# Optimization experiments

Hardware: AMD Instinct MI355X
Metric: run time of the kernel (lower is better)

The kernel has to match this reference:

```python
import jax, jax.numpy as jnp
import numpy as np

B, L, INPUT_DIM = 2, 2048, 512
D_MODEL, N_HEAD, MLP_HIDDEN = 1024, 16, 4096
CONTEXT_LENGTH = 2048
EPS = 1e-5


def _layer_norm(x, w, b):
    mu = jnp.mean(x, axis=-1, keepdims=True)
    var = jnp.mean(jnp.square(x - mu), axis=-1, keepdims=True)
    return (x - mu) * jax.lax.rsqrt(var + EPS) * w + b


def setup_inputs() -> dict:
    key = jax.random.key(0)
    ks = jax.random.split(key, 12)
    s = 0.02
    return {
        "x": jax.random.normal(ks[0], (B, L, INPUT_DIM), dtype=jnp.float32),
        "wte_w": jax.random.normal(ks[1], (INPUT_DIM, D_MODEL), dtype=jnp.float32) * s,
        "wte_b": jnp.zeros((D_MODEL,), dtype=jnp.float32),
        "wpe": jax.random.normal(ks[2], (CONTEXT_LENGTH, D_MODEL), dtype=jnp.float32) * s,
        "ln1_w": jnp.ones((D_MODEL,), dtype=jnp.float32),
        "ln1_b": jnp.zeros((D_MODEL,), dtype=jnp.float32),
        "kq_w": jax.random.normal(ks[3], (D_MODEL, 2 * D_MODEL), dtype=jnp.float32) * s,
        "kq_b": jnp.zeros((2 * D_MODEL,), dtype=jnp.float32),
        "v_w": jax.random.normal(ks[4], (D_MODEL, D_MODEL), dtype=jnp.float32) * s,
        "v_b": jnp.zeros((D_MODEL,), dtype=jnp.float32),
        "ao_w": jax.random.normal(ks[5], (D_MODEL, D_MODEL), dtype=jnp.float32) * s,
        "ao_b": jnp.zeros((D_MODEL,), dtype=jnp.float32),
        "ln2_w": jnp.ones((D_MODEL,), dtype=jnp.float32),
        "ln2_b": jnp.zeros((D_MODEL,), dtype=jnp.float32),
        "fc_w": jax.random.normal(ks[6], (D_MODEL, MLP_HIDDEN), dtype=jnp.float32) * s,
        "fc_b": jnp.zeros((MLP_HIDDEN,), dtype=jnp.float32),
        "proj_w": jax.random.normal(ks[7], (MLP_HIDDEN, INPUT_DIM), dtype=jnp.float32) * s,
        "proj_b": jnp.zeros((INPUT_DIM,), dtype=jnp.float32),
    }


def reference(x, wte_w, wte_b, wpe, ln1_w, ln1_b, kq_w, kq_b, v_w, v_b,
              ao_w, ao_b, ln2_w, ln2_b, fc_w, fc_b, proj_w, proj_b):
    b, l, _ = x.shape
    hd = D_MODEL // N_HEAD
    # token "embedding" (linear) + learnable positional embedding
    h = x @ wte_w + wte_b + wpe[:l]                      # [B, L, D]
    hn = _layer_norm(h, ln1_w, ln1_b)                    # ln_1
    # attention (kq fused linear -> split gives k first, then q)
    kq = hn @ kq_w + kq_b                                # [B, L, 2D]
    k, q = kq[..., :D_MODEL], kq[..., D_MODEL:]
    v = hn @ v_w + v_b
    q = q.reshape(b, l, N_HEAD, hd).transpose(0, 2, 1, 3)  # [B, H, L, hd]
    k = k.reshape(b, l, N_HEAD, hd).transpose(0, 2, 1, 3)
    v = v.reshape(b, l, N_HEAD, hd).transpose(0, 2, 1, 3)
    scale = 1.0 / jnp.sqrt(jnp.asarray(hd, dtype=q.dtype))
    scores = jnp.einsum('bhqd,bhkd->bhqk', q, k) * scale  # [B, H, L, L]
    causal = jnp.tril(jnp.ones((l, l), dtype=bool))
    scores = jnp.where(causal, scores, jnp.asarray(-jnp.inf, dtype=scores.dtype))
    attn = jax.nn.softmax(scores, axis=-1)
    o = jnp.einsum('bhqk,bhkd->bhqd', attn, v)            # [B, H, L, hd]
    o = o.transpose(0, 2, 1, 3).reshape(b, l, D_MODEL)
    o = o @ ao_w + ao_b
    attn_out = hn + o                                     # residual recorded by Block
    xo = _layer_norm(attn_out, ln2_w, ln2_b)              # ln_2
    # MLP head to input_dim (exact GELU, matching torch nn.GELU default)
    out = jax.nn.gelu(xo @ fc_w + fc_b, approximate=False) @ proj_w + proj_b
    return (out, attn_out)
```

## Files before the change

### kernel.cpp

```cpp
#include <hip/hip_runtime.h>
#include <hip/hip_bf16.h>
#include <cmath>

#define D_MODEL   1024
#define N_HEAD    16
#define HEAD_DIM  64
#define SEQ_LEN   2048
#define NBATCH    2
#define M_TOTAL   (NBATCH * SEQ_LEN)
#define IN_DIM    512
#define MLP_HID   4096

typedef __attribute__((ext_vector_type(8))) short short8;
typedef __attribute__((ext_vector_type(4))) short short4v;
typedef __attribute__((ext_vector_type(4))) float floatx4;

typedef const __attribute__((address_space(1))) void* gas_ptr;
typedef __attribute__((address_space(3))) void* las_ptr;

__device__ __forceinline__ void async_copy16(const void* g, void* l) {
  __builtin_amdgcn_global_load_lds((gas_ptr)g, (las_ptr)l, 16, 0, 0);
}


__global__ __launch_bounds__(256) void k_convert_bf16(const float* __restrict__ in,
                                                      __hip_bfloat16* __restrict__ out,
                                                      int n4) {
  int i = blockIdx.x * 256 + threadIdx.x;
  if (i >= n4) return;
  float4 v = ((const float4*)in)[i];
  int base = i * 4;
  out[base + 0] = __float2bfloat16(v.x);
  out[base + 1] = __float2bfloat16(v.y);
  out[base + 2] = __float2bfloat16(v.z);
  out[base + 3] = __float2bfloat16(v.w);
}

__global__ __launch_bounds__(256) void k_reduce_proj(const __hip_bfloat16* __restrict__ part,
                                                     const float* __restrict__ bias,
                                                     float* __restrict__ out) {
  int i = blockIdx.x * 256 + threadIdx.x;
  const size_t SP = (size_t)M_TOTAL * IN_DIM / 4;
  float4 s = ((const float4*)bias)[i & (IN_DIM / 4 - 1)];
#pragma unroll
  for (int j = 0; j < 8; j++) {
    short4v v = ((const short4v*)part)[i + j * SP];
    s.x += __bfloat162float(((const __hip_bfloat16*)&v)[0]);
    s.y += __bfloat162float(((const __hip_bfloat16*)&v)[1]);
    s.z += __bfloat162float(((const __hip_bfloat16*)&v)[2]);
    s.w += __bfloat162float(((const __hip_bfloat16*)&v)[3]);
  }
  ((float4*)out)[i] = s;
}

__global__ __launch_bounds__(256) void k_transpose_bf16(const float* __restrict__ in,
                                                        __hip_bfloat16* __restrict__ out,
                                                        int K, int N) {
  __shared__ float tile[32][33];
  int n0 = blockIdx.x * 32, k0 = blockIdx.y * 32;
  int tx = threadIdx.x & 31, ty = threadIdx.x >> 5;
#pragma unroll
  for (int i = 0; i < 32; i += 8)
    tile[ty + i][tx] = in[(size_t)(k0 + ty + i) * N + n0 + tx];
  __syncthreads();
#pragma unroll
  for (int i = 0; i < 32; i += 8)
    out[(size_t)(n0 + ty + i) * K + k0 + tx] = __float2bfloat16(tile[tx][ty + i]);
}

__global__ __launch_bounds__(256) void k_transpose_v(const __hip_bfloat16* __restrict__ in,
                                                     __hip_bfloat16* __restrict__ out) {
  __shared__ __hip_bfloat16 t[64][72];
  int bh = blockIdx.y;
  int l0 = blockIdx.x * 64;
  in  += (size_t)bh * SEQ_LEN * HEAD_DIM;
  out += (size_t)bh * HEAD_DIM * SEQ_LEN;
  int tx = threadIdx.x & 7, ty = threadIdx.x >> 3;
#pragma unroll
  for (int i = 0; i < 64; i += 32) {
    short8 v = *(const short8*)(in + (size_t)(l0 + ty + i) * HEAD_DIM + tx * 8);
#pragma unroll
    for (int j = 0; j < 8; j++) t[ty + i][tx * 8 + j] = ((__hip_bfloat16*)&v)[j];
  }
  __syncthreads();
#pragma unroll
  for (int i = 0; i < 64; i += 32) {
    int d = ty + i;
    short8 o;
#pragma unroll
    for (int j = 0; j < 8; j++) ((__hip_bfloat16*)&o)[j] = t[tx * 8 + j][d];
    *(short8*)(out + (size_t)d * SEQ_LEN + l0 + tx * 8) = o;
  }
}


__global__ __launch_bounds__(256) void k_ln1_combine(const float* __restrict__ part,
                                                     const float* __restrict__ wb,
                                                     const float* __restrict__ wpe,
                                                     const float* __restrict__ lw,
                                                     const float* __restrict__ lb,
                                                     __hip_bfloat16* __restrict__ out_bf) {
  int row = blockIdx.x;
  int l = row & (SEQ_LEN - 1);
  float4 a = ((const float4*)(part + (size_t)row * D_MODEL))[threadIdx.x];
  float4 c = ((const float4*)(part + (size_t)(M_TOTAL + row) * D_MODEL))[threadIdx.x];
  float4 wb4 = ((const float4*)wb)[threadIdx.x];
  float4 pe4 = ((const float4*)(wpe + (size_t)l * D_MODEL))[threadIdx.x];
  float4 v;
  v.x = a.x + c.x + wb4.x + pe4.x;
  v.y = a.y + c.y + wb4.y + pe4.y;
  v.z = a.z + c.z + wb4.z + pe4.z;
  v.w = a.w + c.w + wb4.w + pe4.w;
  float s  = v.x + v.y + v.z + v.w;
  float sq = v.x * v.x + v.y * v.y + v.z * v.z + v.w * v.w;
#pragma unroll
  for (int o = 1; o < 64; o <<= 1) { s += __shfl_xor(s, o); sq += __shfl_xor(sq, o); }
  __shared__ float ss[4], ssq[4];
  int lane = threadIdx.x & 63, wv = threadIdx.x >> 6;
  if (lane == 0) { ss[wv] = s; ssq[wv] = sq; }
  __syncthreads();
  s  = ss[0] + ss[1] + ss[2] + ss[3];
  sq = ssq[0] + ssq[1] + ssq[2] + ssq[3];
  float mu  = s * (1.f / D_MODEL);
  float var = sq * (1.f / D_MODEL) - mu * mu;
  float rs  = rsqrtf(var + 1e-5f);
  float4 lw4 = ((const float4*)lw)[threadIdx.x];
  float4 lb4 = ((const float4*)lb)[threadIdx.x];
  size_t base = (size_t)row * D_MODEL + threadIdx.x * 4;
  out_bf[base + 0] = __float2bfloat16((v.x - mu) * rs * lw4.x + lb4.x);
  out_bf[base + 1] = __float2bfloat16((v.y - mu) * rs * lw4.y + lb4.y);
  out_bf[base + 2] = __float2bfloat16((v.z - mu) * rs * lw4.z + lb4.z);
  out_bf[base + 3] = __float2bfloat16((v.w - mu) * rs * lw4.w + lb4.w);
}

__global__ __launch_bounds__(256) void k_ln2_combine(const float* __restrict__ part,
                                                     const float* __restrict__ bias,
                                                     const __hip_bfloat16* __restrict__ hn,
                                                     const float* __restrict__ lw,
                                                     const float* __restrict__ lb,
                                                     float* __restrict__ attn_out,
                                                     __hip_bfloat16* __restrict__ out_bf) {
  int row = blockIdx.x;
  float4 a = ((const float4*)(part + (size_t)row * D_MODEL))[threadIdx.x];
  float4 c = ((const float4*)(part + (size_t)(M_TOTAL + row) * D_MODEL))[threadIdx.x];
  float4 b4 = ((const float4*)bias)[threadIdx.x];
  short4v h4 = ((const short4v*)(hn + (size_t)row * D_MODEL))[threadIdx.x];
  float4 v;
  v.x = a.x + c.x + b4.x + __bfloat162float(((const __hip_bfloat16*)&h4)[0]);
  v.y = a.y + c.y + b4.y + __bfloat162float(((const __hip_bfloat16*)&h4)[1]);
  v.z = a.z + c.z + b4.z + __bfloat162float(((const __hip_bfloat16*)&h4)[2]);
  v.w = a.w + c.w + b4.w + __bfloat162float(((const __hip_bfloat16*)&h4)[3]);
  ((float4*)(attn_out + (size_t)row * D_MODEL))[threadIdx.x] = v;
  float s  = v.x + v.y + v.z + v.w;
  float sq = v.x * v.x + v.y * v.y + v.z * v.z + v.w * v.w;
#pragma unroll
  for (int o = 1; o < 64; o <<= 1) { s += __shfl_xor(s, o); sq += __shfl_xor(sq, o); }
  __shared__ float ss[4], ssq[4];
  int lane = threadIdx.x & 63, wv = threadIdx.x >> 6;
  if (lane == 0) { ss[wv] = s; ssq[wv] = sq; }
  __syncthreads();
  s  = ss[0] + ss[1] + ss[2] + ss[3];
  sq = ssq[0] + ssq[1] + ssq[2] + ssq[3];
  float mu  = s * (1.f / D_MODEL);
  float var = sq * (1.f / D_MODEL) - mu * mu;
  float rs  = rsqrtf(var + 1e-5f);
  float4 lw4 = ((const float4*)lw)[threadIdx.x];
  float4 lb4 = ((const float4*)lb)[threadIdx.x];
  size_t base = (size_t)row * D_MODEL + threadIdx.x * 4;
  out_bf[base + 0] = __float2bfloat16((v.x - mu) * rs * lw4.x + lb4.x);
  out_bf[base + 1] = __float2bfloat16((v.y - mu) * rs * lw4.y + lb4.y);
  out_bf[base + 2] = __float2bfloat16((v.z - mu) * rs * lw4.z + lb4.z);
  out_bf[base + 3] = __float2bfloat16((v.w - mu) * rs * lw4.w + lb4.w);
}


struct KQVEpi {
  const float* kq_b; const float* v_b;
  __hip_bfloat16* kb; __hip_bfloat16* qb; __hip_bfloat16* vb;
  __device__ void operator()(int row, int col, float v) const {
    int b = row >> 11, l = row & (SEQ_LEN - 1);
    int which = col >> 10, c = col & (D_MODEL - 1);
    float t = v + ((which == 2) ? v_b[c] : kq_b[col]);
    if (which == 1) t *= 0.125f;
    int head = c >> 6, d = c & 63;
    __hip_bfloat16* dst = (which == 0) ? kb : (which == 1) ? qb : vb;
    dst[(((size_t)(b * N_HEAD + head) * SEQ_LEN) + l) * HEAD_DIM + d] = __float2bfloat16(t);
  }
};

struct FCEpi {
  const float* bias; __hip_bfloat16* act;
  __device__ void operator()(int row, int col, float v) const {
    float t = v + bias[col];
    float g = 0.5f * t * (1.f + erff(t * 0.70710678118654752f));
    act[(size_t)row * MLP_HID + col] = __float2bfloat16(g);
  }
};

struct PartEpi {
  float* part;
  __device__ void operator()(int row, int col, float v) const {
    part[(size_t)blockIdx.z * ((size_t)M_TOTAL * D_MODEL) + (size_t)row * D_MODEL + col] = v;
  }
};

struct PartBf16Epi {
  __hip_bfloat16* part;
  __device__ void operator()(int row, int col, float v) const {
    part[(size_t)blockIdx.z * ((size_t)M_TOTAL * IN_DIM) + (size_t)row * IN_DIM + col] =
        __float2bfloat16(v);
  }
};


#define STAGE_A(BUF, H, KT)                                                       \
  do {                                                                            \
    async_copy16(ga + (size_t)((H) * 128) * K + (KT) * 64,                        \
                 &As[BUF][(tid + (H) * 1024) * 8]);                               \
    async_copy16(ga + (size_t)((H) * 128 + 64) * K + (KT) * 64,                   \
                 &As[BUF][(tid + (H) * 1024 + 512) * 8]);                         \
  } while (0)

#define STAGE_B(BUF, H, KT)                                                       \
  do {                                                                            \
    async_copy16(gb + (size_t)((H) * 128) * K + (KT) * 64,                        \
                 &Bs[BUF][(tid + (H) * 1024) * 8]);                               \
    async_copy16(gb + (size_t)((H) * 128 + 64) * K + (KT) * 64,                   \
                 &Bs[BUF][(tid + (H) * 1024 + 512) * 8]);                         \
  } while (0)

#define MFMA_BLK(IO, JO, BFX)                                                     \
  _Pragma("unroll") for (int i = 0; i < 4; i++) {                                 \
    _Pragma("unroll") for (int j = 0; j < 2; j++) {                               \
      acc[(IO) + i][(JO) + j] = __builtin_amdgcn_mfma_f32_16x16x32_bf16(          \
          af[i][0], BFX[j][0], acc[(IO) + i][(JO) + j], 0, 0, 0);                 \
      acc[(IO) + i][(JO) + j] = __builtin_amdgcn_mfma_f32_16x16x32_bf16(          \
          af[i][1], BFX[j][1], acc[(IO) + i][(JO) + j], 0, 0, 0);                 \
    }                                                                             \
  }

#define GTILE(T, BUF)                                                             \
  {                                                                               \
                                    \
    _Pragma("unroll") for (int i = 0; i < 4; i++) {                               \
      af[i][0] = *(const short8*)&As[BUF][arb[i] + pc0];                          \
      af[i][1] = *(const short8*)&As[BUF][arb[i] + pc1];                          \
    }                                                                             \
    _Pragma("unroll") for (int j = 0; j < 2; j++) {                               \
      bf0[j][0] = *(const short8*)&Bs[BUF][brb[j] + pc0];                         \
      bf0[j][1] = *(const short8*)&Bs[BUF][brb[j] + pc1];                         \
    }                                                                             \
    if ((T) + 1 < nt) { STAGE_A((BUF) ^ 1, 1, (T) + 1); }                         \
    __builtin_amdgcn_s_barrier();                                                 \
    asm volatile("s_waitcnt lgkmcnt(0)" ::: "memory");                            \
    __builtin_amdgcn_s_setprio(1);                                                \
    MFMA_BLK(0, 0, bf0)                                                           \
    __builtin_amdgcn_s_setprio(0);                                                \
    __builtin_amdgcn_s_barrier();                                                 \
                                           \
    _Pragma("unroll") for (int j = 0; j < 2; j++) {                               \
      bf1[j][0] = *(const short8*)&Bs[BUF][brb[j] + 8192 + pc0];                  \
      bf1[j][1] = *(const short8*)&Bs[BUF][brb[j] + 8192 + pc1];                  \
    }                                                                             \
    if ((T) + 2 < nt) { STAGE_A(BUF, 0, (T) + 2); }                               \
    __builtin_amdgcn_s_barrier();                                                 \
    asm volatile("s_waitcnt lgkmcnt(0)" ::: "memory");                            \
    __builtin_amdgcn_s_setprio(1);                                                \
    MFMA_BLK(0, 2, bf1)                                                           \
    __builtin_amdgcn_s_setprio(0);                                                \
    __builtin_amdgcn_s_barrier();                                                 \
                                           \
    _Pragma("unroll") for (int i = 0; i < 4; i++) {                               \
      af[i][0] = *(const short8*)&As[BUF][arb[i] + 8192 + pc0];                   \
      af[i][1] = *(const short8*)&As[BUF][arb[i] + 8192 + pc1];                   \
    }                                                                             \
    if ((T) + 2 < nt) { STAGE_B(BUF, 0, (T) + 2); }                               \
    __builtin_amdgcn_s_barrier();                                                 \
    asm volatile("s_waitcnt lgkmcnt(0)" ::: "memory");                            \
    __builtin_amdgcn_s_setprio(1);                                                \
    MFMA_BLK(4, 0, bf0)                                                           \
    __builtin_amdgcn_s_setprio(0);                                                \
    __builtin_amdgcn_s_barrier();                                                 \
                    \
    if ((T) + 2 < nt) { STAGE_B(BUF, 1, (T) + 2); }                               \
    __builtin_amdgcn_s_setprio(1);                                                \
    MFMA_BLK(4, 2, bf1)                                                           \
    __builtin_amdgcn_s_setprio(0);                                                \
    if ((T) + 2 < nt) {                                                           \
      asm volatile("s_waitcnt vmcnt(6)" ::: "memory");                            \
    } else {                                                                      \
      asm volatile("s_waitcnt vmcnt(0)" ::: "memory");                            \
    }                                                                             \
    __builtin_amdgcn_s_barrier();                                                 \
  }

template <class Epi>
__global__ __launch_bounds__(512, 2) void k_gemm256(const __hip_bfloat16* __restrict__ A,
                                                    const __hip_bfloat16* __restrict__ Bt,
                                                    int M, int N, int K, int Kchunk, Epi epi) {
  (void)M; (void)N;
  __shared__ __align__(16) short As[2][16384];
  __shared__ __align__(16) short Bs[2][16384];
  const int tid  = threadIdx.x;
  const int lane = tid & 63;
  const int w    = tid >> 6;
  const int wr   = w >> 2;
  const int wc   = w & 3;
  const int r    = lane & 15;
  const int quad = lane >> 4;
  const int m0 = blockIdx.y << 8;
  const int n0 = blockIdx.x << 8;
  const int koff = blockIdx.z * Kchunk;
  const int nt = Kchunk >> 6;

  const int sr = tid >> 3;
  const int sc = (tid & 7) ^ (sr & 7);
  const __hip_bfloat16* ga = A  + (size_t)(m0 + sr) * K + sc * 8 + koff;
  const __hip_bfloat16* gb = Bt + (size_t)(n0 + sr) * K + sc * 8 + koff;

  const int pc0 = ((quad    ) ^ (r & 7)) << 3;
  const int pc1 = ((quad + 4) ^ (r & 7)) << 3;
  int arb[4], brb[2];
#pragma unroll
  for (int i = 0; i < 4; i++) arb[i] = ((2 * i + wr) * 16 + r) * 64;
#pragma unroll
  for (int j = 0; j < 2; j++) brb[j] = ((4 * j + wc) * 16 + r) * 64;

  floatx4 acc[8][4];
#pragma unroll
  for (int i = 0; i < 8; i++)
#pragma unroll
    for (int j = 0; j < 4; j++) acc[i][j] = (floatx4){0.f, 0.f, 0.f, 0.f};
  short8 af[4][2], bf0[2][2], bf1[2][2];

  STAGE_A(0, 0, 0);
  STAGE_B(0, 0, 0);
  STAGE_B(0, 1, 0);
  STAGE_A(0, 1, 0);
  if (nt > 1) {
    STAGE_A(1, 0, 1);
    STAGE_B(1, 0, 1);
    STAGE_B(1, 1, 1);
    asm volatile("s_waitcnt vmcnt(6)" ::: "memory");
  } else {
    asm volatile("s_waitcnt vmcnt(0)" ::: "memory");
  }
  __builtin_amdgcn_s_barrier();

  for (int t = 0; t < nt; t += 2) {
    GTILE(t, 0)
    GTILE(t + 1, 1)
  }

#pragma unroll
  for (int i = 0; i < 8; i++) {
    int row = m0 + (2 * i + wr) * 16 + quad * 4;
#pragma unroll
    for (int j = 0; j < 4; j++) {
      int col = n0 + (4 * j + wc) * 16 + r;
#pragma unroll
      for (int tt = 0; tt < 4; tt++) epi(row + tt, col, acc[i][j][tt]);
    }
  }
}


#define PSTR 68

#define STAGE_KV(T, P)                                                         \
  do {                                                                         \
    async_copy16(kp + (size_t)((((T) << 6)) + srow) * HEAD_DIM + sg * 8,       \
                 &Ks[P][tid * 8]);                                             \
    async_copy16(vp + (size_t)srow * SEQ_LEN + ((T) << 6) + sg * 8,            \
                 &Vs[P][tid * 8]);                                             \
  } while (0)

#define ATILE(T, P)                                                            \
  {                                                                            \
    const int ts = (T) << 6;                                                   \
    if (ts < qend) {                                                           \
      _Pragma("unroll") for (int kt = 0; kt < 4; kt++) {                       \
        const int tss = ts + (kt << 4);                                        \
        short4v pk0;                                                           \
        if (tss < qend) {                                                      \
          const int krow = (kt << 4) + r;                                      \
          short8 a0 = *(const short8*)&Ks[P][(krow * 8 + (quad ^ sw)) * 8];    \
          short8 a1 = *(const short8*)&Ks[P][(krow * 8 + ((quad ^ sw) ^ 4)) * 8]; \
          floatx4 s0 = (floatx4){0.f, 0.f, 0.f, 0.f};                          \
          s0 = __builtin_amdgcn_mfma_f32_16x16x32_bf16(a0, qf0, s0, 0, 0, 0);  \
          s0 = __builtin_amdgcn_mfma_f32_16x16x32_bf16(a1, qf1, s0, 0, 0, 0);  \
          if (tss + 15 > qbw) {                                                \
            int off0 = qbw + r - tss;                                          \
            _Pragma("unroll") for (int tt = 0; tt < 4; tt++) {                 \
              int kl = (quad << 2) + tt;                                       \
              if (kl > off0) s0[tt] = -INFINITY;                               \
            }                                                                  \
          }                                                                    \
          _Pragma("unroll") for (int tt = 0; tt < 4; tt++) {                   \
            float e0 = __expf(s0[tt]); ls0 += e0;                              \
            ((__hip_bfloat16*)&pk0)[tt] = __float2bfloat16(e0);                \
          }                                                                    \
        } else {                                                               \
          pk0 = (short4v){0, 0, 0, 0};                                         \
        }                                                                      \
        *(short4v*)(pw + r * PSTR + (kt << 4) + (quad << 2)) = pk0;            \
      }                                                                        \
      __builtin_amdgcn_s_setprio(1);                                           \
      _Pragma("unroll") for (int c = 0; c < 2; c++) {                          \
        short8 pb0 = *(const short8*)(pw + r * PSTR + (c << 5) + (quad << 3)); \
        _Pragma("unroll") for (int fd = 0; fd < 4; fd++) {                     \
          const int vrow = (fd << 4) + r;                                      \
          short8 va = *(const short8*)&Vs[P][(vrow * 8 + (((c << 2) + quad) ^ sw)) * 8]; \
          of[fd] = __builtin_amdgcn_mfma_f32_16x16x32_bf16(va, pb0, of[fd], 0, 0, 0); \
        }                                                                      \
      }                                                                        \
      __builtin_amdgcn_s_setprio(0);                                           \
    }                                                                          \
    __builtin_amdgcn_s_barrier();                                              \
    if ((T) + 2 < ktiles) {                                                    \
      STAGE_KV((T) + 2, P);                                                    \
      asm volatile("s_waitcnt vmcnt(2)" ::: "memory");                         \
    } else {                                                                   \
      asm volatile("s_waitcnt vmcnt(0)" ::: "memory");                         \
    }                                                                          \
    __builtin_amdgcn_s_barrier();                                              \
    __builtin_amdgcn_sched_barrier(0);                                         \
  }

__global__ __launch_bounds__(512, 4) void k_flash_attn(const __hip_bfloat16* __restrict__ kb,
                                                       const __hip_bfloat16* __restrict__ qb,
                                                       const __hip_bfloat16* __restrict__ vtb,
                                                       __hip_bfloat16* __restrict__ ob) {
  __shared__ __align__(16) short Ks[2][64 * 64];
  __shared__ __align__(16) short Vs[2][64 * 64];
  __shared__ __align__(16) __hip_bfloat16 Pb[8][16 * PSTR];
  const int tid  = threadIdx.x;
  const int lane = tid & 63;
  const int w    = tid >> 6;
  const int r    = lane & 15;
  const int quad = lane >> 4;
  const int sw   = r & 7;
  const int bh    = blockIdx.x & 31;
  const int strip = (SEQ_LEN / 128 - 1) - (blockIdx.x >> 5);
  const int qb0   = strip << 7;
  const int qbw   = qb0 + (w << 4);
  const int qend  = qbw + 16;
  const int b = bh >> 4, h = bh & (N_HEAD - 1);

  const __hip_bfloat16* qp = qb  + ((size_t)bh * SEQ_LEN + qbw) * HEAD_DIM;
  const __hip_bfloat16* kp = kb  + (size_t)bh * SEQ_LEN * HEAD_DIM;
  const __hip_bfloat16* vp = vtb + (size_t)bh * HEAD_DIM * SEQ_LEN;
  __hip_bfloat16* pw = &Pb[w][0];

  short8 qf0 = *(const short8*)(qp + r * HEAD_DIM + quad * 8);
  short8 qf1 = *(const short8*)(qp + r * HEAD_DIM + quad * 8 + 32);

  floatx4 of[4];
#pragma unroll
  for (int i = 0; i < 4; i++) of[i] = (floatx4){0.f, 0.f, 0.f, 0.f};
  float ls0 = 0.f;

  const int srow = tid >> 3;
  const int sg = (tid & 7) ^ (srow & 7);

  const int ktiles = (qb0 + 128) >> 6;
  STAGE_KV(0, 0);
  STAGE_KV(1, 1);
  asm volatile("s_waitcnt vmcnt(2)" ::: "memory");
  __builtin_amdgcn_s_barrier();
  __builtin_amdgcn_sched_barrier(0);

  for (int t = 0; t < ktiles; t += 2) {
    ATILE(t, 0)
    ATILE(t + 1, 1)
  }

  ls0 += __shfl_xor(ls0, 16); ls0 += __shfl_xor(ls0, 32);
  float inv0 = 1.f / ls0;

  size_t orow = ((size_t)b * SEQ_LEN + qbw + r) * D_MODEL + (size_t)h * HEAD_DIM;
#pragma unroll
  for (int fd = 0; fd < 4; fd++) {
    short4v o4;
#pragma unroll
    for (int tt = 0; tt < 4; tt++)
      ((__hip_bfloat16*)&o4)[tt] = __float2bfloat16(of[fd][tt] * inv0);
    *(short4v*)(ob + orow + fd * 16 + quad * 4) = o4;
  }
}


extern "C" void kernel_launch(void* const* d_in, const int* in_sizes, int n_in,
                              void* d_out, int out_size, void* d_ws, size_t ws_size,
                              hipStream_t stream) {
  (void)in_sizes; (void)n_in; (void)out_size; (void)ws_size;
  const float* x      = (const float*)d_in[0];
  const float* wte_w  = (const float*)d_in[1];
  const float* wte_b  = (const float*)d_in[2];
  const float* wpe    = (const float*)d_in[3];
  const float* ln1_w  = (const float*)d_in[4];
  const float* ln1_b  = (const float*)d_in[5];
  const float* kq_w   = (const float*)d_in[6];
  const float* kq_b   = (const float*)d_in[7];
  const float* v_w    = (const float*)d_in[8];
  const float* v_b    = (const float*)d_in[9];
  const float* ao_w   = (const float*)d_in[10];
  const float* ao_b   = (const float*)d_in[11];
  const float* ln2_w  = (const float*)d_in[12];
  const float* ln2_b  = (const float*)d_in[13];
  const float* fc_w   = (const float*)d_in[14];
  const float* fc_b   = (const float*)d_in[15];
  const float* proj_w = (const float*)d_in[16];
  const float* proj_b = (const float*)d_in[17];

  float* out0     = (float*)d_out;
  float* attn_out = out0 + (size_t)M_TOTAL * IN_DIM;

  char* ws = (char*)d_ws;
  const size_t MB8 = (size_t)M_TOTAL * D_MODEL * 2;
  __hip_bfloat16* wT    = (__hip_bfloat16*)ws;
  __hip_bfloat16* x_bf  = (__hip_bfloat16*)(ws + 8 * 1048576);
  char* R1              = ws + 12 * 1048576;
  float* embed_part     = (float*)R1;
  float* ao_part        = (float*)R1;
  __hip_bfloat16* act   = (__hip_bfloat16*)R1;
  __hip_bfloat16* k_bf  = (__hip_bfloat16*)(ws + 44 * 1048576);
  __hip_bfloat16* q_bf  = (__hip_bfloat16*)(ws + 52 * 1048576);
  __hip_bfloat16* v_bf  = (__hip_bfloat16*)(ws + 60 * 1048576);
  __hip_bfloat16* vt_bf = (__hip_bfloat16*)(ws + 68 * 1048576);
  __hip_bfloat16* o_bf  = (__hip_bfloat16*)(ws + 76 * 1048576);
  __hip_bfloat16* hn_bf = (__hip_bfloat16*)(ws + 84 * 1048576);
  __hip_bfloat16* xo_bf = k_bf;
  __hip_bfloat16* proj_part = k_bf;
  (void)MB8;

  k_convert_bf16<<<(M_TOTAL * IN_DIM / 4 + 255) / 256, 256, 0, stream>>>(x, x_bf, M_TOTAL * IN_DIM / 4);

  k_transpose_bf16<<<dim3(D_MODEL / 32, IN_DIM / 32), 256, 0, stream>>>(wte_w, wT, IN_DIM, D_MODEL);
  {
    dim3 grid(D_MODEL / 256, M_TOTAL / 256, 2);
    k_gemm256<PartEpi><<<grid, 512, 0, stream>>>(x_bf, wT, M_TOTAL, D_MODEL, IN_DIM, IN_DIM / 2,
                                                 PartEpi{embed_part});
  }

  k_ln1_combine<<<M_TOTAL, 256, 0, stream>>>(embed_part, wte_b, wpe, ln1_w, ln1_b, hn_bf);

  k_transpose_bf16<<<dim3(2 * D_MODEL / 32, D_MODEL / 32), 256, 0, stream>>>(kq_w, wT, D_MODEL, 2 * D_MODEL);
  k_transpose_bf16<<<dim3(D_MODEL / 32, D_MODEL / 32), 256, 0, stream>>>(v_w, wT + (size_t)2 * D_MODEL * D_MODEL, D_MODEL, D_MODEL);
  {
    dim3 grid(3 * D_MODEL / 256, M_TOTAL / 256, 1);
    k_gemm256<KQVEpi><<<grid, 512, 0, stream>>>(hn_bf, wT, M_TOTAL, 3 * D_MODEL, D_MODEL, D_MODEL,
                                                KQVEpi{kq_b, v_b, k_bf, q_bf, v_bf});
  }
  k_transpose_v<<<dim3(SEQ_LEN / 64, NBATCH * N_HEAD), 256, 0, stream>>>(v_bf, vt_bf);

  k_flash_attn<<<(SEQ_LEN / 128) * 32, 512, 0, stream>>>(k_bf, q_bf, vt_bf, o_bf);

  k_transpose_bf16<<<dim3(D_MODEL / 32, D_MODEL / 32), 256, 0, stream>>>(ao_w, wT, D_MODEL, D_MODEL);
  {
    dim3 grid(D_MODEL / 256, M_TOTAL / 256, 2);
    k_gemm256<PartEpi><<<grid, 512, 0, stream>>>(o_bf, wT, M_TOTAL, D_MODEL, D_MODEL, D_MODEL / 2,
                                                 PartEpi{ao_part});
  }

  k_ln2_combine<<<M_TOTAL, 256, 0, stream>>>(ao_part, ao_b, hn_bf, ln2_w, ln2_b, attn_out, xo_bf);

  k_transpose_bf16<<<dim3(MLP_HID / 32, D_MODEL / 32), 256, 0, stream>>>(fc_w, wT, D_MODEL, MLP_HID);
  {
    dim3 grid(MLP_HID / 256, M_TOTAL / 256, 1);
    k_gemm256<FCEpi><<<grid, 512, 0, stream>>>(xo_bf, wT, M_TOTAL, MLP_HID, D_MODEL, D_MODEL,
                                               FCEpi{fc_b, act});
  }

  k_transpose_bf16<<<dim3(IN_DIM / 32, MLP_HID / 32), 256, 0, stream>>>(proj_w, wT, MLP_HID, IN_DIM);
  {
    dim3 grid(IN_DIM / 256, M_TOTAL / 256, 8);
    k_gemm256<PartBf16Epi><<<grid, 512, 0, stream>>>(act, wT, M_TOTAL, IN_DIM, MLP_HID, MLP_HID / 8,
                                                     PartBf16Epi{proj_part});
  }
  k_reduce_proj<<<M_TOTAL * IN_DIM / 4 / 256, 256, 0, stream>>>(proj_part, proj_b, out0);
}
```

Baseline: 406.7 us.

## Merge weight transposes and input conversion into one prep kernel; use 128-tile GEMM

Result: faster. 386.8 us (-4.9%).

```diff
diff --git a/kernel.cpp b/kernel.cpp
--- a/kernel.cpp
+++ b/kernel.cpp
@@ -23,17 +23,46 @@
 }
 
 
-__global__ __launch_bounds__(256) void k_convert_bf16(const float* __restrict__ in,
-                                                      __hip_bfloat16* __restrict__ out,
-                                                      int n4) {
-  int i = blockIdx.x * 256 + threadIdx.x;
-  if (i >= n4) return;
-  float4 v = ((const float4*)in)[i];
-  int base = i * 4;
-  out[base + 0] = __float2bfloat16(v.x);
-  out[base + 1] = __float2bfloat16(v.y);
-  out[base + 2] = __float2bfloat16(v.z);
-  out[base + 3] = __float2bfloat16(v.w);
+__global__ __launch_bounds__(256) void k_prep(const float* __restrict__ wte_w,
+                                              const float* __restrict__ kq_w,
+                                              const float* __restrict__ v_w,
+                                              const float* __restrict__ ao_w,
+                                              const float* __restrict__ fc_w,
+                                              const float* __restrict__ proj_w,
+                                              const float* __restrict__ x,
+                                              __hip_bfloat16* __restrict__ wT,
+                                              __hip_bfloat16* __restrict__ x_bf) {
+  const int bid = blockIdx.x;
+  const float* in; __hip_bfloat16* out; int K, N, local;
+  if (bid < 512)        { in = wte_w;  out = wT;           K = IN_DIM;  N = D_MODEL;     local = bid;        }
+  else if (bid < 2560)  { in = kq_w;   out = wT +  524288; K = D_MODEL; N = 2 * D_MODEL; local = bid - 512;  }
+  else if (bid < 3584)  { in = v_w;    out = wT + 2621440; K = D_MODEL; N = D_MODEL;     local = bid - 2560; }
+  else if (bid < 4608)  { in = ao_w;   out = wT + 3670016; K = D_MODEL; N = D_MODEL;     local = bid - 3584; }
+  else if (bid < 8704)  { in = fc_w;   out = wT + 4718592; K = D_MODEL; N = MLP_HID;     local = bid - 4608; }
+  else if (bid < 10752) { in = proj_w; out = wT + 8912896; K = MLP_HID; N = IN_DIM;      local = bid - 8704; }
+  else {
+    int i = (bid - 10752) * 256 + threadIdx.x;
+    float4 v = ((const float4*)x)[i];
+    short4v o;
+    ((__hip_bfloat16*)&o)[0] = __float2bfloat16(v.x);
+    ((__hip_bfloat16*)&o)[1] = __float2bfloat16(v.y);
+    ((__hip_bfloat16*)&o)[2] = __float2bfloat16(v.z);
+    ((__hip_bfloat16*)&o)[3] = __float2bfloat16(v.w);
+    ((short4v*)x_bf)[i] = o;
+    return;
+  }
+  __shared__ float tile[32][33];
+  const int ntx = N >> 5;
+  const int bx = local % ntx, by = local / ntx;
+  const int n0 = bx * 32, k0 = by * 32;
+  const int tx = threadIdx.x & 31, ty = threadIdx.x >> 5;
+#pragma unroll
+  for (int i = 0; i < 32; i += 8)
+    tile[ty + i][tx] = in[(size_t)(k0 + ty + i) * N + n0 + tx];
+  __syncthreads();
+#pragma unroll
+  for (int i = 0; i < 32; i += 8)
+    out[(size_t)(n0 + ty + i) * K + k0 + tx] = __float2bfloat16(tile[tx][ty + i]);
 }
 
 __global__ __launch_bounds__(256) void k_reduce_proj(const __hip_bfloat16* __restrict__ part,
@@ -51,21 +80,6 @@
     s.w += __bfloat162float(((const __hip_bfloat16*)&v)[3]);
   }
   ((float4*)out)[i] = s;
-}
-
-__global__ __launch_bounds__(256) void k_transpose_bf16(const float* __restrict__ in,
-                                                        __hip_bfloat16* __restrict__ out,
-                                                        int K, int N) {
-  __shared__ float tile[32][33];
-  int n0 = blockIdx.x * 32, k0 = blockIdx.y * 32;
-  int tx = threadIdx.x & 31, ty = threadIdx.x >> 5;
-#pragma unroll
-  for (int i = 0; i < 32; i += 8)
-    tile[ty + i][tx] = in[(size_t)(k0 + ty + i) * N + n0 + tx];
-  __syncthreads();
-#pragma unroll
-  for (int i = 0; i < 32; i += 8)
-    out[(size_t)(n0 + ty + i) * K + k0 + tx] = __float2bfloat16(tile[tx][ty + i]);
 }
 
 __global__ __launch_bounds__(256) void k_transpose_v(const __hip_bfloat16* __restrict__ in,
@@ -213,6 +227,93 @@
 };
 
 
+template <class Epi>
+__global__ __launch_bounds__(256) void k_gemm(const __hip_bfloat16* __restrict__ A,
+                                              const __hip_bfloat16* __restrict__ Bt,
+                                              int M, int N, int K, int Kchunk, Epi epi) {
+  __shared__ __align__(16) short As[128 * 64];
+  __shared__ __align__(16) short Bs[128 * 64];
+  const int tid  = threadIdx.x;
+  const int lane = tid & 63;
+  const int w    = tid >> 6;
+  const int wm   = (w >> 1) << 6;
+  const int wn   = (w & 1) << 6;
+  const int r    = lane & 15;
+  const int quad = lane >> 4;
+  const int m0 = blockIdx.y << 7;
+  const int n0 = blockIdx.x << 7;
+  const int koff = blockIdx.z * Kchunk;
+
+  const __hip_bfloat16* pa[4];
+  const __hip_bfloat16* pb[4];
+#pragma unroll
+  for (int j = 0; j < 4; j++) {
+    int s = tid + j * 256;
+    int row = s >> 3;
+    int c = (s & 7) ^ (row & 7);
+    pa[j] = A  + (size_t)(m0 + row) * K + (c << 3) + koff;
+    pb[j] = Bt + (size_t)(n0 + row) * K + (c << 3) + koff;
+  }
+
+  floatx4 acc[4][4];
+#pragma unroll
+  for (int i = 0; i < 4; i++)
+#pragma unroll
+    for (int j = 0; j < 4; j++) acc[i][j] = (floatx4){0.f, 0.f, 0.f, 0.f};
+
+  int aoff[2][4], boff[2][4];
+#pragma unroll
+  for (int kk = 0; kk < 2; kk++)
+#pragma unroll
+    for (int i = 0; i < 4; i++) {
+      int pc = ((quad + (kk << 2)) ^ (r & 7)) << 3;
+      aoff[kk][i] = (wm + i * 16 + r) * 64 + pc;
+      boff[kk][i] = (wn + i * 16 + r) * 64 + pc;
+    }
+
+  for (int k0 = 0; k0 < Kchunk; k0 += 64) {
+    __syncthreads();
+#pragma unroll
+    for (int j = 0; j < 4; j++) {
+      async_copy16(pa[j] + k0, &As[(tid + j * 256) * 8]);
+      async_copy16(pb[j] + k0, &Bs[(tid + j * 256) * 8]);
+    }
+    __syncthreads();
+#pragma unroll
+    for (int kk = 0; kk < 2; kk++) {
+      short8 fa[4], fb[4];
+#pragma unroll
+      for (int i = 0; i < 4; i++) {
+        fa[i] = *(const short8*)&As[aoff[kk][i]];
+        fb[i] = *(const short8*)&Bs[boff[kk][i]];
+      }
+#pragma unroll
+      for (int i = 0; i < 4; i++)
+#pragma unroll
+        for (int j = 0; j < 4; j++)
+          acc[i][j] = __builtin_amdgcn_mfma_f32_16x16x32_bf16(fa[i], fb[j], acc[i][j], 0, 0, 0);
+    }
+  }
+
+#pragma unroll
+  for (int i = 0; i < 4; i++)
+#pragma unroll
+    for (int j = 0; j < 4; j++) {
+      int row = m0 + wm + i * 16 + quad * 4;
+      int col = n0 + wn + j * 16 + r;
+#pragma unroll
+      for (int t = 0; t < 4; t++) epi(row + t, col, acc[i][j][t]);
+    }
+}
+
+template <class Epi>
+static void launch_gemm(const __hip_bfloat16* A, const __hip_bfloat16* Bt,
+                        int M, int N, int K, Epi epi, hipStream_t s) {
+  dim3 grid(N / 128, M / 128, 1);
+  k_gemm<Epi><<<grid, 256, 0, s>>>(A, Bt, M, N, K, K, epi);
+}
+
+
 #define STAGE_A(BUF, H, KT)                                                       \
   do {                                                                            \
     async_copy16(ga + (size_t)((H) * 128) * K + (KT) * 64,                        \
@@ -241,7 +342,6 @@
 
 #define GTILE(T, BUF)                                                             \
   {                                                                               \
-                                    \
     _Pragma("unroll") for (int i = 0; i < 4; i++) {                               \
       af[i][0] = *(const short8*)&As[BUF][arb[i] + pc0];                          \
       af[i][1] = *(const short8*)&As[BUF][arb[i] + pc1];                          \
@@ -257,7 +357,6 @@
     MFMA_BLK(0, 0, bf0)                                                           \
     __builtin_amdgcn_s_setprio(0);                                                \
     __builtin_amdgcn_s_barrier();                                                 \
-                                           \
     _Pragma("unroll") for (int j = 0; j < 2; j++) {                               \
       bf1[j][0] = *(const short8*)&Bs[BUF][brb[j] + 8192 + pc0];                  \
       bf1[j][1] = *(const short8*)&Bs[BUF][brb[j] + 8192 + pc1];                  \
@@ -269,7 +368,6 @@
     MFMA_BLK(0, 2, bf1)                                                           \
     __builtin_amdgcn_s_setprio(0);                                                \
     __builtin_amdgcn_s_barrier();                                                 \
-                                           \
     _Pragma("unroll") for (int i = 0; i < 4; i++) {                               \
       af[i][0] = *(const short8*)&As[BUF][arb[i] + 8192 + pc0];                   \
       af[i][1] = *(const short8*)&As[BUF][arb[i] + 8192 + pc1];                   \
@@ -281,7 +379,6 @@
     MFMA_BLK(4, 0, bf0)                                                           \
     __builtin_amdgcn_s_setprio(0);                                                \
     __builtin_amdgcn_s_barrier();                                                 \
-                    \
     if ((T) + 2 < nt) { STAGE_B(BUF, 1, (T) + 2); }                               \
     __builtin_amdgcn_s_setprio(1);                                                \
     MFMA_BLK(4, 2, bf1)                                                           \
@@ -517,66 +614,57 @@
   float* attn_out = out0 + (size_t)M_TOTAL * IN_DIM;
 
   char* ws = (char*)d_ws;
-  const size_t MB8 = (size_t)M_TOTAL * D_MODEL * 2;
   __hip_bfloat16* wT    = (__hip_bfloat16*)ws;
-  __hip_bfloat16* x_bf  = (__hip_bfloat16*)(ws + 8 * 1048576);
-  char* R1              = ws + 12 * 1048576;
+  __hip_bfloat16* x_bf  = (__hip_bfloat16*)(ws + 22 * 1048576);
+  char* R1              = ws + 26 * 1048576;
   float* embed_part     = (float*)R1;
   float* ao_part        = (float*)R1;
   __hip_bfloat16* act   = (__hip_bfloat16*)R1;
-  __hip_bfloat16* k_bf  = (__hip_bfloat16*)(ws + 44 * 1048576);
-  __hip_bfloat16* q_bf  = (__hip_bfloat16*)(ws + 52 * 1048576);
-  __hip_bfloat16* v_bf  = (__hip_bfloat16*)(ws + 60 * 1048576);
-  __hip_bfloat16* vt_bf = (__hip_bfloat16*)(ws + 68 * 1048576);
-  __hip_bfloat16* o_bf  = (__hip_bfloat16*)(ws + 76 * 1048576);
-  __hip_bfloat16* hn_bf = (__hip_bfloat16*)(ws + 84 * 1048576);
+  __hip_bfloat16* k_bf  = (__hip_bfloat16*)(ws + 58 * 1048576);
+  __hip_bfloat16* q_bf  = (__hip_bfloat16*)(ws + 66 * 1048576);
+  __hip_bfloat16* v_bf  = (__hip_bfloat16*)(ws + 74 * 1048576);
+  __hip_bfloat16* vt_bf = (__hip_bfloat16*)(ws + 82 * 1048576);
+  __hip_bfloat16* o_bf  = v_bf;
+  __hip_bfloat16* hn_bf = (__hip_bfloat16*)(ws + 90 * 1048576);
   __hip_bfloat16* xo_bf = k_bf;
   __hip_bfloat16* proj_part = k_bf;
-  (void)MB8;
-
-  k_convert_bf16<<<(M_TOTAL * IN_DIM / 4 + 255) / 256, 256, 0, stream>>>(x, x_bf, M_TOTAL * IN_DIM / 4);
-
-  k_transpose_bf16<<<dim3(D_MODEL / 32, IN_DIM / 32), 256, 0, stream>>>(wte_w, wT, IN_DIM, D_MODEL);
+
+  __hip_bfloat16* wteT  = wT;
+  __hip_bfloat16* kqvT  = wT +  524288;
+  __hip_bfloat16* aoT   = wT + 3670016;
+  __hip_bfloat16* fcT   = wT + 4718592;
+  __hip_bfloat16* projT = wT + 8912896;
+
+  k_prep<<<12800, 256, 0, stream>>>(wte_w, kq_w, v_w, ao_w, fc_w, proj_w, x, wT, x_bf);
+
   {
-    dim3 grid(D_MODEL / 256, M_TOTAL / 256, 2);
-    k_gemm256<PartEpi><<<grid, 512, 0, stream>>>(x_bf, wT, M_TOTAL, D_MODEL, IN_DIM, IN_DIM / 2,
-                                                 PartEpi{embed_part});
+    dim3 grid(D_MODEL / 128, M_TOTAL / 128, 2);
+    k_gemm<PartEpi><<<grid, 256, 0, stream>>>(x_bf, wteT, M_TOTAL, D_MODEL, IN_DIM, IN_DIM / 2,
+                                              PartEpi{embed_part});
   }
 
   k_ln1_combine<<<M_TOTAL, 256, 0, stream>>>(embed_part, wte_b, wpe, ln1_w, ln1_b, hn_bf);
 
-  k_transpose_bf16<<<dim3(2 * D_MODEL / 32, D_MODEL / 32), 256, 0, stream>>>(kq_w, wT, D_MODEL, 2 * D_MODEL);
-  k_transpose_bf16<<<dim3(D_MODEL / 32, D_MODEL / 32), 256, 0, stream>>>(v_w, wT + (size_t)2 * D_MODEL * D_MODEL, D_MODEL, D_MODEL);
+  launch_gemm(hn_bf, kqvT, M_TOTAL, 3 * D_MODEL, D_MODEL,
+              KQVEpi{kq_b, v_b, k_bf, q_bf, v_bf}, stream);
+  k_transpose_v<<<dim3(SEQ_LEN / 64, NBATCH * N_HEAD), 256, 0, stream>>>(v_bf, vt_bf);
+
+  k_flash_attn<<<(SEQ_LEN / 128) * 32, 512, 0, stream>>>(k_bf, q_bf, vt_bf, o_bf);
+
   {
-    dim3 grid(3 * D_MODEL / 256, M_TOTAL / 256, 1);
-    k_gemm256<KQVEpi><<<grid, 512, 0, stream>>>(hn_bf, wT, M_TOTAL, 3 * D_MODEL, D_MODEL, D_MODEL,
-                                                KQVEpi{kq_b, v_b, k_bf, q_bf, v_bf});
-  }
-  k_transpose_v<<<dim3(SEQ_LEN / 64, NBATCH * N_HEAD), 256, 0, stream>>>(v_bf, vt_bf);
-
-  k_flash_attn<<<(SEQ_LEN / 128) * 32, 512, 0, stream>>>(k_bf, q_bf, vt_bf, o_bf);
-
-  k_transpose_bf16<<<dim3(D_MODEL / 32, D_MODEL / 32), 256, 0, stream>>>(ao_w, wT, D_MODEL, D_MODEL);
-  {
-    dim3 grid(D_MODEL / 256, M_TOTAL / 256, 2);
-    k_gemm256<PartEpi><<<grid, 512, 0, stream>>>(o_bf, wT, M_TOTAL, D_MODEL, D_MODEL, D_MODEL / 2,
-                                                 PartEpi{ao_part});
+    dim3 grid(D_MODEL / 128, M_TOTAL / 128, 2);
+    k_gemm<PartEpi><<<grid, 256, 0, stream>>>(o_bf, aoT, M_TOTAL, D_MODEL, D_MODEL, D_MODEL / 2,
+                                              PartEpi{ao_part});
   }
 
   k_ln2_combine<<<M_TOTAL, 256, 0, stream>>>(ao_part, ao_b, hn_bf, ln2_w, ln2_b, attn_out, xo_bf);
 
-  k_transpose_bf16<<<dim3(MLP_HID / 32, D_MODEL / 32), 256, 0, stream>>>(fc_w, wT, D_MODEL, MLP_HID);
-  {
-    dim3 grid(MLP_HID / 256, M_TOTAL / 256, 1);
-    k_gemm256<FCEpi><<<grid, 512, 0, stream>>>(xo_bf, wT, M_TOTAL, MLP_HID, D_MODEL, D_MODEL,
-                                               FCEpi{fc_b, act});
-  }
-
-  k_transpose_bf16<<<dim3(IN_DIM / 32, MLP_HID / 32), 256, 0, stream>>>(proj_w, wT, MLP_HID, IN_DIM);
+  launch_gemm(xo_bf, fcT, M_TOTAL, MLP_HID, D_MODEL, FCEpi{fc_b, act}, stream);
+
   {
     dim3 grid(IN_DIM / 256, M_TOTAL / 256, 8);
-    k_gemm256<PartBf16Epi><<<grid, 512, 0, stream>>>(act, wT, M_TOTAL, IN_DIM, MLP_HID, MLP_HID / 8,
-                                                     PartBf16Epi{proj_part});
+    k_gemm256<PartBf16Epi><<<grid, 512, 0, stream>>>(act, projT, M_TOTAL, IN_DIM, MLP_HID,
+                                                     MLP_HID / 8, PartBf16Epi{proj_part});
   }
   k_reduce_proj<<<M_TOTAL * IN_DIM / 4 / 256, 256, 0, stream>>>(proj_part, proj_b, out0);
 }
```
